# Optimization experiments

Hardware: AMD Instinct MI355X
Metric: run time of the kernel (lower is better)

Reference implementation:

```python
import jax, jax.numpy as jnp
import numpy as np

# dims: 64 graphs x 1024 nodes, 32768 edges/graph, 256 feats, 64 pools/graph
B, NPG, EPG, F, C = 64, 1024, 32768, 256, 64
N, E = B * NPG, B * EPG


def setup_inputs() -> dict:
    key = jax.random.key(0)
    k1, k2, k3, k4, k5 = jax.random.split(key, 5)
    x = jax.random.normal(k1, (N, F), jnp.float32)
    # within-graph edges (block structure, as in real batched graphs)
    src = jax.random.randint(k2, (B, EPG), 0, NPG, dtype=jnp.int32)
    dst = jax.random.randint(k3, (B, EPG), 0, NPG, dtype=jnp.int32)
    off = (jnp.arange(B, dtype=jnp.int32) * NPG)[:, None]
    edge_index = jnp.stack([(src + off).reshape(-1), (dst + off).reshape(-1)], 0)
    edge_weight = jax.random.uniform(k4, (E,), jnp.float32)
    batch = jnp.repeat(jnp.arange(B, dtype=jnp.int32), NPG)
    batch_ptr = jnp.arange(B + 1, dtype=jnp.int32) * NPG
    # pooling_net stand-in: linear d_feat -> num_pools
    W = jax.random.normal(k5, (F, C), jnp.float32) * 0.05
    b = jnp.zeros((C,), jnp.float32)
    return dict(x=x, edge_index=edge_index, edge_weight=edge_weight,
                batch=batch, batch_ptr=batch_ptr, W=W, b=b)


def reference(x, edge_index, edge_weight, batch, batch_ptr, W, b):
    num_batches = batch_ptr.shape[0] - 1
    Cp = W.shape[1]  # num_pools_per_graph
    logits = x @ W + b                       # pooling_net(x, edge_index)
    sm = jax.nn.softmax(logits, axis=-1)     # [N, C]
    c = jnp.argmax(sm, axis=-1)              # hard cluster per node [N]
    p = jnp.take_along_axis(sm, c[:, None], axis=-1)[:, 0]
    # straight-through nonzero value of s (==1.0 in forward value)
    v = 1.0 - jax.lax.stop_gradient(p) + p
    gcl = batch * Cp + c                     # global cluster id [N]
    K = num_batches * Cp
    # out = S^T x  -> segment reduce over nodes by global cluster
    out = jax.ops.segment_sum(v[:, None] * x, gcl, num_segments=K)  # [K, F]
    # out_adj = S^T A S  (block diagonal over graphs): per-edge scatter
    src, dst = edge_index[0], edge_index[1]
    ci, cj = c[src], c[dst]
    gb = batch[src]
    flat = gb * (Cp * Cp) + ci * Cp + cj
    contrib = edge_weight * v[src] * v[dst]
    out_adj = jax.ops.segment_sum(contrib, flat, num_segments=num_batches * Cp * Cp)
    # dense block-diagonal index set (torch returns coalesced nonzeros;
    # jit needs static shapes, so we enumerate all within-graph pool pairs)
    idx = jnp.arange(num_batches * Cp * Cp, dtype=jnp.int32)
    bb, rem = idx // (Cp * Cp), idx % (Cp * Cp)
    out_edge_index = jnp.stack([bb * Cp + rem // Cp, bb * Cp + rem % Cp], 0)
    # link_loss = ||A - S S^T||_F / E  via exact decomposition
    a2 = jnp.sum(edge_weight * edge_weight)
    ap = jnp.sum(jnp.where(gcl[src] == gcl[dst], contrib, 0.0))
    vs2 = jax.ops.segment_sum(v * v, gcl, num_segments=K)
    p2 = jnp.sum(vs2 * vs2)
    link_loss = jnp.sqrt(jnp.maximum(a2 - 2.0 * ap + p2, 0.0)) / edge_index.shape[1]
    batch_out = jnp.repeat(jnp.arange(num_batches, dtype=jnp.int32), Cp)
    batch_ptr_out = jnp.arange(num_batches + 1, dtype=jnp.int32) * Cp
    return (out, out_edge_index, out_adj, link_loss, jnp.float32(0.0),
            batch_out, batch_ptr_out)
```

## Files before the change

kernel.cpp:

```cpp
#include <hip/hip_runtime.h>
#include <cstdint>
#include <cstddef>

typedef __attribute__((ext_vector_type(8))) short short8;
typedef __attribute__((ext_vector_type(4))) float f32x4;

#define GLOAD_LDS16(gsrc, ldst) \
    __builtin_amdgcn_global_load_lds( \
        (const __attribute__((address_space(1))) void*)(gsrc), \
        (__attribute__((address_space(3))) void*)(ldst), 16, 0, 0)

namespace {
constexpr int kN    = 65536;
constexpr int kF    = 256;
constexpr int kC    = 64;
constexpr int kNPG  = 1024;
constexpr int kB    = 64;
constexpr int kE    = 2097152;
constexpr int kK    = kB * kC;

constexpr size_t OFF_OUT  = 0;
constexpr size_t OFF_EIDX = (size_t)kK * kF;
constexpr size_t OFF_ADJ  = OFF_EIDX + 2ull*kB*kC*kC;
constexpr size_t OFF_LL   = OFF_ADJ + (size_t)kB*kC*kC;
constexpr size_t OFF_Z    = OFF_LL + 1;
constexpr size_t OFF_BOUT = OFF_Z + 1;
constexpr size_t OFF_BPTR = OFF_BOUT + kK;

constexpr size_t WS_C    = 0;
constexpr size_t WS_V    = 262144;
constexpr size_t WS_VS2  = 524288;
constexpr size_t WS_A2   = 540672;
constexpr size_t WS_PERM = 544768;
constexpr size_t WS_STRT = 806912;
constexpr size_t WS_WTH  = 1048576;
constexpr size_t WS_WTL  = 1081344;
constexpr size_t WS_PADJ = 544768;

__device__ __forceinline__ unsigned short bf16_rn(float f)
{
    const unsigned int b = __float_as_uint(f);
    return (unsigned short)((b + 0x7fffu + ((b >> 16) & 1u)) >> 16);
}
}

__global__ __launch_bounds__(256) void k_const(float* __restrict__ out,
                                               const float* __restrict__ Wm,
                                               unsigned short* __restrict__ wth,
                                               unsigned short* __restrict__ wtl)
{
    const int i = blockIdx.x * 256 + threadIdx.x;
    constexpr int E2 = 2 * kB * kC * kC;
    constexpr int B3 = E2 + kK + kB + 1;
    if (i < E2) {
        const int half = i >= kB*kC*kC;
        const int idx  = half ? i - kB*kC*kC : i;
        const int bb = idx >> 12, rem = idx & 4095;
        const int val = half ? bb*kC + (rem & 63) : bb*kC + (rem >> 6);
        out[OFF_EIDX + i] = (float)val;
    } else if (i < E2 + kK) {
        const int j = i - E2;
        out[OFF_BOUT + j] = (float)(j >> 6);
    } else if (i < B3) {
        const int j = i - (E2 + kK);
        out[OFF_BPTR + j] = (float)(j * kC);
    } else if (i < B3 + 16384) {
        const int j = i - B3;
        const int c = j >> 8, k = j & 255;
        const float w = Wm[(size_t)k*kC + c];
        const unsigned short h = bf16_rn(w);
        const float hf = __uint_as_float((unsigned int)h << 16);
        wth[j] = h;
        wtl[j] = bf16_rn(w - hf);
    }
}

__global__ __launch_bounds__(256) void k_logits(
    const float* __restrict__ x, const unsigned short* __restrict__ wth,
    const unsigned short* __restrict__ wtl, const float* __restrict__ bv,
    int* __restrict__ carr, float* __restrict__ varr)
{
    __shared__ float xs[2][128 * 32];
    const int tid  = threadIdx.x;
    const int lane = tid & 63;
    const int w    = tid >> 6;
    const int nbase = blockIdx.x * 128;
    const int l15  = lane & 15;
    const int kgrp = lane >> 4;

    const int snode = lane >> 3;
    const int soff  = (lane & 7) * 4;

    f32x4 acc[2][4];
#pragma unroll
    for (int mt = 0; mt < 2; ++mt)
#pragma unroll
        for (int nt = 0; nt < 4; ++nt)
            acc[mt][nt] = f32x4{0.f, 0.f, 0.f, 0.f};

#pragma unroll
    for (int i = 0; i < 4; ++i) {
        const int g = w*4 + i;
        const float* src = x + (size_t)(nbase + g*8 + snode)*kF + soff;
        GLOAD_LDS16(src, &xs[0][g*256]);
    }

#pragma unroll 1
    for (int c = 0; c < 8; ++c) {
        if (c < 7) {
#pragma unroll
            for (int i = 0; i < 4; ++i) {
                const int g = w*4 + i;
                const float* src = x + (size_t)(nbase + g*8 + snode)*kF
                                     + (c+1)*32 + soff;
                GLOAD_LDS16(src, &xs[(c+1) & 1][g*256]);
            }
            asm volatile("s_waitcnt vmcnt(4)" ::: "memory");
        } else {
            asm volatile("s_waitcnt vmcnt(0)" ::: "memory");
        }
        __syncthreads();

        const float* __restrict__ xb = &xs[c & 1][0];
        const int koff = c*32 + kgrp*8;
        short8 bh[4], bl[4];
#pragma unroll
        for (int nt = 0; nt < 4; ++nt) {
            const size_t wo = (size_t)(nt*16 + l15)*kF + koff;
            bh[nt] = *reinterpret_cast<const short8*>(wth + wo);
            bl[nt] = *reinterpret_cast<const short8*>(wtl + wo);
        }
#pragma unroll
        for (int mt = 0; mt < 2; ++mt) {
            const int a = (w*32 + mt*16 + l15)*32 + kgrp*8;
            const float4 xa = *reinterpret_cast<const float4*>(&xb[a]);
            const float4 xc = *reinterpret_cast<const float4*>(&xb[a+4]);
            const float xv[8] = {xa.x, xa.y, xa.z, xa.w,
                                 xc.x, xc.y, xc.z, xc.w};
            short8 ah, al;
#pragma unroll
            for (int j = 0; j < 8; ++j) {
                const unsigned short h = bf16_rn(xv[j]);
                const float hf = __uint_as_float((unsigned int)h << 16);
                ah[j] = (short)h;
                al[j] = (short)bf16_rn(xv[j] - hf);
            }
#pragma unroll
            for (int nt = 0; nt < 4; ++nt) {
                acc[mt][nt] = __builtin_amdgcn_mfma_f32_16x16x32_bf16(
                    ah, bh[nt], acc[mt][nt], 0, 0, 0);
                acc[mt][nt] = __builtin_amdgcn_mfma_f32_16x16x32_bf16(
                    al, bh[nt], acc[mt][nt], 0, 0, 0);
                acc[mt][nt] = __builtin_amdgcn_mfma_f32_16x16x32_bf16(
                    ah, bl[nt], acc[mt][nt], 0, 0, 0);
                acc[mt][nt] = __builtin_amdgcn_mfma_f32_16x16x32_bf16(
                    al, bl[nt], acc[mt][nt], 0, 0, 0);
            }
        }
        __syncthreads();
    }

#pragma unroll
    for (int mt = 0; mt < 2; ++mt) {
#pragma unroll
        for (int nt = 0; nt < 4; ++nt) {
            const float b = bv[nt*16 + l15];
#pragma unroll
            for (int r = 0; r < 4; ++r) acc[mt][nt][r] += b;
        }
#pragma unroll
        for (int r = 0; r < 4; ++r) {
            float m = acc[mt][0][r]; int ci = l15;
#pragma unroll
            for (int nt = 1; nt < 4; ++nt) {
                if (acc[mt][nt][r] > m) { m = acc[mt][nt][r]; ci = nt*16 + l15; }
            }
#pragma unroll
            for (int off = 1; off < 16; off <<= 1) {
                const float om = __shfl_xor(m, off);
                const int   oc = __shfl_xor(ci, off);
                if (om > m || (om == m && oc < ci)) { m = om; ci = oc; }
            }
            float s = 0.f;
#pragma unroll
            for (int nt = 0; nt < 4; ++nt) s += expf(acc[mt][nt][r] - m);
#pragma unroll
            for (int off = 1; off < 16; off <<= 1) s += __shfl_xor(s, off);
            if (l15 == r) {
                const float p = 1.0f / s;
                const int n = nbase + w*32 + mt*16 + kgrp*4 + r;
                carr[n] = ci;
                varr[n] = (1.0f - p) + p;
            }
        }
    }
}

__global__ __launch_bounds__(1024) void k_sort(
    const int* __restrict__ carr, int* __restrict__ perm,
    int* __restrict__ startc)
{
    __shared__ int hist[16][64];
    __shared__ int startS[65];
    const int g = blockIdx.x;
    const int tid = threadIdx.x;
    const int w = tid >> 6, lane = tid & 63;
    const int c = carr[g*kNPG + tid];
    hist[tid >> 6][tid & 63] = 0;
    __syncthreads();
    unsigned long long mm = ~0ull;
#pragma unroll
    for (int b = 0; b < 6; ++b) {
        const unsigned long long bal = __ballot((c >> b) & 1);
        mm &= ((c >> b) & 1) ? bal : ~bal;
    }
    const unsigned long long ltmask =
        (lane == 0) ? 0ull : (~0ull >> (64 - lane));
    const int rank_in_wave = __popcll(mm & ltmask);
    const int leader = __ffsll((unsigned long long)mm) - 1;
    if (lane == leader) hist[w][c] = __popcll(mm);
    __syncthreads();
    if (w == 0) {
        int tot = 0;
#pragma unroll
        for (int i = 0; i < 16; ++i) tot += hist[i][lane];
        int pre = tot;
#pragma unroll
        for (int off = 1; off < 64; off <<= 1) {
            const int t = __shfl_up(pre, off);
            if (lane >= off) pre += t;
        }
        startS[lane + 1] = pre;
        if (lane == 0) startS[0] = 0;
    }
    __syncthreads();
    int before = startS[c];
    for (int i = 0; i < w; ++i) before += hist[i][c];
    perm[g*kNPG + before + rank_in_wave] = g*kNPG + tid;
    if (tid < 65) startc[g*65 + tid] = startS[tid];
}

__global__ __launch_bounds__(1024) void k_pool_x(
    const float* __restrict__ x, const int* __restrict__ perm,
    const int* __restrict__ startc, const float* __restrict__ varr,
    float* __restrict__ out, float* __restrict__ vs2)
{
    const int tid  = threadIdx.x;
    const int g    = blockIdx.x >> 3;
    const int fh   = blockIdx.x & 7;
    const int w    = tid >> 6;
    const int lane = tid & 63;
    const int q    = lane & 7;
    const int sub  = lane >> 3;
    const int fbase = fh*32 + q*4;
#pragma unroll
    for (int cc = 0; cc < 4; ++cc) {
        const int c = w*4 + cc;
        const int s = startc[g*65 + c];
        const int e = startc[g*65 + c + 1];
        float ax = 0.f, ay = 0.f, az = 0.f, aw = 0.f, v2 = 0.f;
        for (int base = s + sub; base < e; base += 8) {
            const int n = perm[(size_t)g*kNPG + base];
            const float v = varr[n];
            const float4 xv = *reinterpret_cast<const float4*>(
                x + (size_t)n*kF + fbase);
            ax = fmaf(v, xv.x, ax); ay = fmaf(v, xv.y, ay);
            az = fmaf(v, xv.z, az); aw = fmaf(v, xv.w, aw);
            v2 = fmaf(v, v, v2);
        }
#pragma unroll
        for (int off = 8; off < 64; off <<= 1) {
            ax += __shfl_xor(ax, off); ay += __shfl_xor(ay, off);
            az += __shfl_xor(az, off); aw += __shfl_xor(aw, off);
            v2 += __shfl_xor(v2, off);
        }
        if (sub == 0) {
            const float4 o = {ax, ay, az, aw};
            *reinterpret_cast<float4*>(
                out + OFF_OUT + (size_t)(g*kC + c)*kF + fbase) = o;
        }
        if (fh == 0 && lane == 0) vs2[g*kC + c] = v2;
    }
}

__global__ __launch_bounds__(1024) void k_adj(
    const int* __restrict__ ei, const float* __restrict__ ew,
    const int* __restrict__ carr, const float* __restrict__ varr,
    float* __restrict__ padj, float* __restrict__ a2p)
{
    __shared__ float adj[kC*kC];
    __shared__ float vls[kNPG];
    __shared__ int   cls[kNPG];
    __shared__ float wred[16];
    const int tid = threadIdx.x;
    const int bid = blockIdx.x;
    const int g   = bid >> 2;
    for (int i = tid; i < kC*kC; i += 1024) adj[i] = 0.f;
    vls[tid] = varr[g*kNPG + tid];
    cls[tid] = carr[g*kNPG + tid];
    __syncthreads();
    const int e0 = bid * 8192;
    float a2l = 0.f;
#pragma unroll
    for (int it = 0; it < 8; ++it) {
        const int e  = e0 + it*1024 + tid;
        const int sn = ei[e]      & (kNPG - 1);
        const int dn = ei[kE + e] & (kNPG - 1);
        const float wv = ew[e];
        a2l += wv * wv;
        atomicAdd(&adj[cls[sn]*kC + cls[dn]], wv * vls[sn] * vls[dn]);
    }
    __syncthreads();
#pragma unroll
    for (int r = 0; r < 4; ++r) {
        const int lin = r*1024 + tid;
        padj[(size_t)bid*4096 + lin] = adj[lin];
    }
#pragma unroll
    for (int off = 32; off > 0; off >>= 1) a2l += __shfl_down(a2l, off);
    if ((tid & 63) == 0) wred[tid >> 6] = a2l;
    __syncthreads();
    if (tid == 0) {
        float s = 0.f;
#pragma unroll
        for (int wv = 0; wv < 16; ++wv) s += wred[wv];
        a2p[bid] = s;
    }
}

__global__ __launch_bounds__(256) void k_adj_merge(
    const float* __restrict__ padj, float* __restrict__ out)
{
    const int id = blockIdx.x*256 + threadIdx.x;
    const int g = id >> 12, idx = id & 4095;
    float s = 0.f;
#pragma unroll
    for (int sp = 0; sp < 4; ++sp) s += padj[(size_t)(g*4 + sp)*4096 + idx];
    out[OFF_ADJ + id] = s;
}

__global__ __launch_bounds__(256) void k_final(
    const float* __restrict__ vs2, const float* __restrict__ a2p,
    float* __restrict__ out)
{
    const int tid = threadIdx.x;
    float p2l = 0.f, apl = 0.f;
#pragma unroll
    for (int r = 0; r < 16; ++r) {
        const int k = r*256 + tid;
        const float t = vs2[k];
        p2l += t*t;
        const int g = k >> 6, cc = k & 63;
        apl += out[OFF_ADJ + (size_t)g*4096 + cc*65];
    }
    float a2l = a2p[tid];
#pragma unroll
    for (int off = 32; off > 0; off >>= 1) {
        p2l += __shfl_down(p2l, off);
        apl += __shfl_down(apl, off);
        a2l += __shfl_down(a2l, off);
    }
    __shared__ float red[3][4];
    if ((tid & 63) == 0) {
        red[0][tid>>6] = p2l; red[1][tid>>6] = apl; red[2][tid>>6] = a2l;
    }
    __syncthreads();
    if (tid == 0) {
        const float p2 = red[0][0]+red[0][1]+red[0][2]+red[0][3];
        const float ap = red[1][0]+red[1][1]+red[1][2]+red[1][3];
        const float a2 = red[2][0]+red[2][1]+red[2][2]+red[2][3];
        const float val = a2 - 2.0f*ap + p2;
        out[OFF_LL] = sqrtf(fmaxf(val, 0.f)) / (float)kE;
        out[OFF_Z]  = 0.0f;
    }
}

extern "C" void kernel_launch(void* const* d_in, const int* in_sizes, int n_in,
                              void* d_out, int out_size, void* d_ws, size_t ws_size,
                              hipStream_t stream)
{
    const float* x  = (const float*)d_in[0];
    const int*   ei = (const int*)d_in[1];
    const float* ew = (const float*)d_in[2];
    const float* Wm = (const float*)d_in[5];
    const float* bv = (const float*)d_in[6];
    float* out = (float*)d_out;
    char*  ws  = (char*)d_ws;
    int*   carr  = (int*)(ws + WS_C);
    float* varr  = (float*)(ws + WS_V);
    float* vs2   = (float*)(ws + WS_VS2);
    float* a2p   = (float*)(ws + WS_A2);
    int*   perm  = (int*)(ws + WS_PERM);
    int*   strt  = (int*)(ws + WS_STRT);
    unsigned short* wth = (unsigned short*)(ws + WS_WTH);
    unsigned short* wtl = (unsigned short*)(ws + WS_WTL);
    float* padj  = (float*)(ws + WS_PADJ);

    k_const    <<<2129, 256, 0, stream>>>(out, Wm, wth, wtl);
    k_logits   <<<512,  256, 0, stream>>>(x, wth, wtl, bv, carr, varr);
    k_sort     <<<64,  1024, 0, stream>>>(carr, perm, strt);
    k_pool_x   <<<512, 1024, 0, stream>>>(x, perm, strt, varr, out, vs2);
    k_adj      <<<256, 1024, 0, stream>>>(ei, ew, carr, varr, padj, a2p);
    k_adj_merge<<<1024, 256, 0, stream>>>(padj, out);
    k_final    <<<1,    256, 0, stream>>>(vs2, a2p, out);
}
```

Measured before the change: 79.50 us.

## Pre-permute W into MFMA fragments, swizzle LDS x tile, split adjacency scatter

k_const now writes the bf16 hi/lo parts of W in MFMA fragment order, so each lane in k_logits fetches its B operand with one contiguous 16-byte load per tile instead of a strided gather. The x tile staged into LDS is XOR-swizzled by row on both the global-to-LDS write and the fragment read, to cut LDS bank conflicts on the float4 reads. k_adj goes from 4 to 8 blocks per graph (512 blocks, 4096 edges each), with the merge and the final a2 reduction changed to sum 8 partials. The trade-offs are more partial adjacency matrices to zero, write and merge, plus slightly more index arithmetic.

```diff
diff --git a/kernel.cpp b/kernel.cpp
--- a/kernel.cpp
+++ b/kernel.cpp
@@ -33,8 +33,8 @@
 constexpr size_t WS_A2   = 540672;
 constexpr size_t WS_PERM = 544768;
 constexpr size_t WS_STRT = 806912;
-constexpr size_t WS_WTH  = 1048576;
-constexpr size_t WS_WTL  = 1081344;
+constexpr size_t WS_WPH  = 1048576;
+constexpr size_t WS_WPL  = 1081344;
 constexpr size_t WS_PADJ = 544768;
 
 __device__ __forceinline__ unsigned short bf16_rn(float f)
@@ -46,8 +46,8 @@
 
 __global__ __launch_bounds__(256) void k_const(float* __restrict__ out,
                                                const float* __restrict__ Wm,
-                                               unsigned short* __restrict__ wth,
-                                               unsigned short* __restrict__ wtl)
+                                               unsigned short* __restrict__ wph,
+                                               unsigned short* __restrict__ wpl)
 {
     const int i = blockIdx.x * 256 + threadIdx.x;
     constexpr int E2 = 2 * kB * kC * kC;
@@ -64,20 +64,26 @@
     } else if (i < B3) {
         const int j = i - (E2 + kK);
         out[OFF_BPTR + j] = (float)(j * kC);
-    } else if (i < B3 + 16384) {
-        const int j = i - B3;
-        const int c = j >> 8, k = j & 255;
-        const float w = Wm[(size_t)k*kC + c];
-        const unsigned short h = bf16_rn(w);
-        const float hf = __uint_as_float((unsigned int)h << 16);
-        wth[j] = h;
-        wtl[j] = bf16_rn(w - hf);
+    } else if (i < B3 + 32768) {
+        const int j  = (i - B3) & 16383;
+        const int lo = (i - B3) >= 16384;
+        const int jj = j & 7, lane = (j >> 3) & 63;
+        const int nt = (j >> 9) & 3, ks = j >> 11;
+        const float wv = Wm[(size_t)(ks*32 + (lane>>4)*8 + jj)*kC
+                            + nt*16 + (lane & 15)];
+        const unsigned short h = bf16_rn(wv);
+        if (!lo) {
+            wph[j] = h;
+        } else {
+            const float hf = __uint_as_float((unsigned int)h << 16);
+            wpl[j] = bf16_rn(wv - hf);
+        }
     }
 }
 
 __global__ __launch_bounds__(256) void k_logits(
-    const float* __restrict__ x, const unsigned short* __restrict__ wth,
-    const unsigned short* __restrict__ wtl, const float* __restrict__ bv,
+    const float* __restrict__ x, const unsigned short* __restrict__ wph,
+    const unsigned short* __restrict__ wpl, const float* __restrict__ bv,
     int* __restrict__ carr, float* __restrict__ varr)
 {
     __shared__ float xs[2][128 * 32];
@@ -89,7 +95,7 @@
     const int kgrp = lane >> 4;
 
     const int snode = lane >> 3;
-    const int soff  = (lane & 7) * 4;
+    const int sfo   = (((lane & 7) ^ snode)) * 4;
 
     f32x4 acc[2][4];
 #pragma unroll
@@ -101,7 +107,7 @@
 #pragma unroll
     for (int i = 0; i < 4; ++i) {
         const int g = w*4 + i;
-        const float* src = x + (size_t)(nbase + g*8 + snode)*kF + soff;
+        const float* src = x + (size_t)(nbase + g*8 + snode)*kF + sfo;
         GLOAD_LDS16(src, &xs[0][g*256]);
     }
 
@@ -112,7 +118,7 @@
             for (int i = 0; i < 4; ++i) {
                 const int g = w*4 + i;
                 const float* src = x + (size_t)(nbase + g*8 + snode)*kF
-                                     + (c+1)*32 + soff;
+                                     + (c+1)*32 + sfo;
                 GLOAD_LDS16(src, &xs[(c+1) & 1][g*256]);
             }
             asm volatile("s_waitcnt vmcnt(4)" ::: "memory");
@@ -122,19 +128,22 @@
         __syncthreads();
 
         const float* __restrict__ xb = &xs[c & 1][0];
-        const int koff = c*32 + kgrp*8;
         short8 bh[4], bl[4];
 #pragma unroll
         for (int nt = 0; nt < 4; ++nt) {
-            const size_t wo = (size_t)(nt*16 + l15)*kF + koff;
-            bh[nt] = *reinterpret_cast<const short8*>(wth + wo);
-            bl[nt] = *reinterpret_cast<const short8*>(wtl + wo);
+            const size_t wo = ((size_t)(c*4 + nt)*64 + lane) * 8;
+            bh[nt] = *reinterpret_cast<const short8*>(wph + wo);
+            bl[nt] = *reinterpret_cast<const short8*>(wpl + wo);
         }
 #pragma unroll
         for (int mt = 0; mt < 2; ++mt) {
-            const int a = (w*32 + mt*16 + l15)*32 + kgrp*8;
-            const float4 xa = *reinterpret_cast<const float4*>(&xb[a]);
-            const float4 xc = *reinterpret_cast<const float4*>(&xb[a+4]);
+            const int row = w*32 + mt*16 + l15;
+            const int sA  = ((kgrp*2)     ^ (row & 7)) * 4;
+            const int sC  = ((kgrp*2 + 1) ^ (row & 7)) * 4;
+            const float4 xa = *reinterpret_cast<const float4*>(
+                &xb[row*32 + sA]);
+            const float4 xc = *reinterpret_cast<const float4*>(
+                &xb[row*32 + sC]);
             const float xv[8] = {xa.x, xa.y, xa.z, xa.w,
                                  xc.x, xc.y, xc.z, xc.w};
             short8 ah, al;
@@ -294,15 +303,15 @@
     __shared__ float wred[16];
     const int tid = threadIdx.x;
     const int bid = blockIdx.x;
-    const int g   = bid >> 2;
+    const int g   = bid >> 3;
     for (int i = tid; i < kC*kC; i += 1024) adj[i] = 0.f;
     vls[tid] = varr[g*kNPG + tid];
     cls[tid] = carr[g*kNPG + tid];
     __syncthreads();
-    const int e0 = bid * 8192;
+    const int e0 = bid * 4096;
     float a2l = 0.f;
 #pragma unroll
-    for (int it = 0; it < 8; ++it) {
+    for (int it = 0; it < 4; ++it) {
         const int e  = e0 + it*1024 + tid;
         const int sn = ei[e]      & (kNPG - 1);
         const int dn = ei[kE + e] & (kNPG - 1);
@@ -335,7 +344,7 @@
     const int g = id >> 12, idx = id & 4095;
     float s = 0.f;
 #pragma unroll
-    for (int sp = 0; sp < 4; ++sp) s += padj[(size_t)(g*4 + sp)*4096 + idx];
+    for (int sp = 0; sp < 8; ++sp) s += padj[(size_t)(g*8 + sp)*4096 + idx];
     out[OFF_ADJ + id] = s;
 }
 
@@ -353,7 +362,7 @@
         const int g = k >> 6, cc = k & 63;
         apl += out[OFF_ADJ + (size_t)g*4096 + cc*65];
     }
-    float a2l = a2p[tid];
+    float a2l = a2p[tid] + a2p[tid + 256];
 #pragma unroll
     for (int off = 32; off > 0; off >>= 1) {
         p2l += __shfl_down(p2l, off);
@@ -392,15 +401,15 @@
     float* a2p   = (float*)(ws + WS_A2);
     int*   perm  = (int*)(ws + WS_PERM);
     int*   strt  = (int*)(ws + WS_STRT);
-    unsigned short* wth = (unsigned short*)(ws + WS_WTH);
-    unsigned short* wtl = (unsigned short*)(ws + WS_WTL);
+    unsigned short* wph = (unsigned short*)(ws + WS_WPH);
+    unsigned short* wpl = (unsigned short*)(ws + WS_WPL);
     float* padj  = (float*)(ws + WS_PADJ);
 
-    k_const    <<<2129, 256, 0, stream>>>(out, Wm, wth, wtl);
-    k_logits   <<<512,  256, 0, stream>>>(x, wth, wtl, bv, carr, varr);
+    k_const    <<<2193, 256, 0, stream>>>(out, Wm, wph, wpl);
+    k_logits   <<<512,  256, 0, stream>>>(x, wph, wpl, bv, carr, varr);
     k_sort     <<<64,  1024, 0, stream>>>(carr, perm, strt);
     k_pool_x   <<<512, 1024, 0, stream>>>(x, perm, strt, varr, out, vs2);
-    k_adj      <<<256, 1024, 0, stream>>>(ei, ew, carr, varr, padj, a2p);
+    k_adj      <<<512, 1024, 0, stream>>>(ei, ew, carr, varr, padj, a2p);
     k_adj_merge<<<1024, 256, 0, stream>>>(padj, out);
     k_final    <<<1,    256, 0, stream>>>(vs2, a2p, out);
 }
```

After: 75.55 us. 5.0% less time.
